# Kernel optimization log

Hardware: AMD Instinct MI355X
Metric: run time of the kernel (lower is better)

Reference implementation:

```python
import jax, jax.numpy as jnp
import numpy as np

N = 100000      # nodes
E = 1600000     # edges
IN_DIM = 256
HID = 64
NCLS = 32


def setup_inputs() -> dict:
    key = jax.random.key(0)
    ks = jax.random.split(key, 7)
    features = jax.random.normal(ks[0], (N, IN_DIM), dtype=jnp.float32)
    hidden_prev = jax.random.normal(ks[1], (N, HID), dtype=jnp.float32)
    adj_indices = jax.random.randint(ks[2], (2, E), 0, N, dtype=jnp.int32)
    # torch.rand init, scaled by 0.1 to keep activations numerically sane
    W0 = jax.random.uniform(ks[3], (IN_DIM, HID), dtype=jnp.float32) * 0.1
    W1 = jax.random.uniform(ks[4], (HID, HID), dtype=jnp.float32) * 0.1
    W2 = jax.random.uniform(ks[5], (HID, NCLS), dtype=jnp.float32) * 0.1
    att_w = jax.random.uniform(ks[6], (2 * HID, 1), dtype=jnp.float32) * 0.1
    return {"features": features, "hidden_prev": hidden_prev,
            "adj_indices": adj_indices, "W0": W0, "W1": W1, "W2": W2,
            "att_w": att_w}


def _edge_softmax(scores, rows, n):
    # sparse softmax over dim=1 of an NxN COO: normalize per source row
    m = jax.ops.segment_max(scores, rows, num_segments=n)
    ex = jnp.exp(scores - m[rows])
    s = jax.ops.segment_sum(ex, rows, num_segments=n)
    return ex / s[rows]


def _compute_attention(hfeat, adj_indices, att_w):
    src, dst = adj_indices[0], adj_indices[1]
    h = hfeat.shape[1]
    # cat(f_src, f_dst) @ att_w == f_src @ w_a + f_dst @ w_b ; project per-node
    proj_a = hfeat @ att_w[:h, 0]   # [N]
    proj_b = hfeat @ att_w[h:, 0]   # [N]
    scores = jax.nn.leaky_relu(proj_a[src] + proj_b[dst])  # [E]
    return _edge_softmax(scores, src, hfeat.shape[0])


def _spmm(att_vals, adj_indices, x):
    # out[i] = sum_{(i,j) in E} att * x[j]
    src, dst = adj_indices[0], adj_indices[1]
    return jax.ops.segment_sum(att_vals[:, None] * x[dst], src,
                               num_segments=x.shape[0])


def reference(features, hidden_prev, adj_indices, W0, W1, W2, att_w):
    att = _compute_attention(hidden_prev, adj_indices, att_w)  # [E]
    h = features
    for W in (W0, W1, W2):
        h = jax.nn.elu(_spmm(att, adj_indices, h @ W))
    return jax.nn.log_softmax(h, axis=1)
```

## Files before the change

kernel.cpp:

```cpp
#include <hip/hip_runtime.h>
#include <math.h>

#define HIDN 64
#define NCLS_K 32
#define INDIM 256
#define BSHIFT 7
#define MAXBUCK 1024
#define BUCK_CAP 4096
#define DSTBITS 17
#define DSTMASK ((1 << DSTBITS) - 1)
#define SCB 512

typedef unsigned int uint;
typedef unsigned short ushort;
typedef __attribute__((ext_vector_type(8))) short short8v;
typedef __attribute__((ext_vector_type(4))) float f32x4;

__device__ inline ushort f2bf(float f) {
  uint u = __float_as_uint(f);
  return (ushort)((u + 0x7FFFu + ((u >> 16) & 1u)) >> 16);
}
__device__ inline float bf2f(ushort h) { return __uint_as_float(((uint)h) << 16); }

__global__ __launch_bounds__(256) void proj_kernel(const float* __restrict__ hid,
    const float* __restrict__ attw, float* __restrict__ pa, float* __restrict__ pb, int n) {
  int wid  = (blockIdx.x * blockDim.x + threadIdx.x) >> 6;
  int lane = threadIdx.x & 63;
  if (wid >= n) return;
  float v = hid[(size_t)wid * HIDN + lane];
  float a = v * attw[lane];
  float b = v * attw[HIDN + lane];
  #pragma unroll
  for (int off = 32; off >= 1; off >>= 1) {
    a += __shfl_xor(a, off, 64);
    b += __shfl_xor(b, off, 64);
  }
  if (lane == 0) { pa[wid] = a; pb[wid] = b; }
}

__global__ __launch_bounds__(256) void hist2(const int* __restrict__ src,
    int* __restrict__ hmatT, int e, int nb, int nper) {
  __shared__ int h[MAXBUCK];
  int lo = blockIdx.x * nper;
  int hi = min(e, lo + nper);
  for (int j = threadIdx.x; j < nb; j += 256) h[j] = 0;
  __syncthreads();
  for (int i = lo + threadIdx.x; i < hi; i += 256)
    atomicAdd(&h[src[i] >> BSHIFT], 1);
  __syncthreads();
  for (int j = threadIdx.x; j < nb; j += 256)
    hmatT[(size_t)j * SCB + blockIdx.x] = h[j];
}

__global__ __launch_bounds__(256) void col_scan(int* __restrict__ hmatT,
    int* __restrict__ bcnt, int nb) {
  constexpr int PER = SCB / 64;
  int wv = blockIdx.x * 4 + (threadIdx.x >> 6);
  if (wv >= nb) return;
  int lane = threadIdx.x & 63;
  int* col = hmatT + (size_t)wv * SCB + lane * PER;
  int v[PER];
  int s = 0;
  #pragma unroll
  for (int q = 0; q < PER; ++q) { v[q] = col[q]; s += v[q]; }
  int x = s;
  #pragma unroll
  for (int off = 1; off < 64; off <<= 1) {
    int t = __shfl_up(x, off, 64);
    if (lane >= off) x += t;
  }
  int pre = x - s;
  #pragma unroll
  for (int q = 0; q < PER; ++q) { int t = v[q]; col[q] = pre; pre += t; }
  if (lane == 63) bcnt[wv] = pre;
}

__global__ __launch_bounds__(1024) void scan_buckets(const int* __restrict__ bcnt,
    int* __restrict__ bbase, int* __restrict__ rowp, int nb, int n, int e) {
  __shared__ int sm[1024];
  int tid = threadIdx.x;
  int v = (tid < nb) ? bcnt[tid] : 0;
  sm[tid] = v;
  __syncthreads();
  for (int off = 1; off < 1024; off <<= 1) {
    int t = (tid >= off) ? sm[tid - off] : 0;
    __syncthreads();
    sm[tid] += t;
    __syncthreads();
  }
  if (tid < nb) bbase[tid] = sm[tid] - v;
  if (tid == 0) { bbase[nb] = e; rowp[n] = e; }
}

__global__ __launch_bounds__(256) void scatter2(const int* __restrict__ src,
    const int* __restrict__ dst, const int* __restrict__ hmatT,
    const int* __restrict__ bbase, int* __restrict__ pairs, int e, int nb, int nper) {
  __shared__ int h[MAXBUCK];
  int lo = blockIdx.x * nper;
  int hi = min(e, lo + nper);
  for (int j = threadIdx.x; j < nb; j += 256)
    h[j] = bbase[j] + hmatT[(size_t)j * SCB + blockIdx.x];
  __syncthreads();
  for (int i = lo + threadIdx.x; i < hi; i += 256) {
    int s = src[i];
    int pos = atomicAdd(&h[s >> BSHIFT], 1);
    pairs[pos] = ((s & 127) << DSTBITS) | dst[i];
  }
}

__global__ __launch_bounds__(256) void build_csr(const int* __restrict__ pairs,
    const int* __restrict__ bbase, int* __restrict__ rowp,
    int* __restrict__ dstc, int n) {
  __shared__ int hist[128];
  __shared__ int cur[128];
  __shared__ int ord[BUCK_CAP];
  int b = blockIdx.x;
  int tid = threadIdx.x;
  int base = bbase[b];
  int m = bbase[b + 1] - base;
  if (tid < 128) hist[tid] = 0;
  __syncthreads();
  for (int i = tid; i < m; i += 256)
    atomicAdd(&hist[pairs[base + i] >> DSTBITS], 1);
  __syncthreads();
  int own = (tid < 128) ? hist[tid] : 0;
  for (int off = 1; off < 128; off <<= 1) {
    int t = (tid < 128 && tid >= off) ? hist[tid - off] : 0;
    __syncthreads();
    if (tid < 128) hist[tid] += t;
    __syncthreads();
  }
  if (tid < 128) {
    int excl = hist[tid] - own;
    cur[tid] = excl;
    int s = (b << BSHIFT) + tid;
    if (s < n) rowp[s] = base + excl;
  }
  __syncthreads();
  for (int i = tid; i < m; i += 256) {
    int key = pairs[base + i];
    int pos = atomicAdd(&cur[key >> DSTBITS], 1);
    ord[pos] = key;
  }
  __syncthreads();
  for (int i = tid; i < m; i += 256) dstc[base + i] = ord[i];
}

__device__ inline int wave_sort64(int key, int lane) {
  #pragma unroll
  for (int k = 2; k <= 64; k <<= 1) {
    #pragma unroll
    for (int j = k >> 1; j > 0; j >>= 1) {
      int p = __shfl_xor(key, j, 64);
      bool up    = ((lane & k) == 0);
      bool lower = ((lane & j) == 0);
      int mn = min(key, p), mx = max(key, p);
      key = (lower == up) ? mn : mx;
    }
  }
  return key;
}

__global__ __launch_bounds__(256) void att_softmax(const float* __restrict__ pa,
    const float* __restrict__ pb, int* __restrict__ dstc,
    const int* __restrict__ rowp, ushort* __restrict__ attb, int n) {
  int wid  = (blockIdx.x * blockDim.x + threadIdx.x) >> 6;
  int lane = threadIdx.x & 63;
  if (wid >= n) return;
  int start = rowp[wid], end = rowp[wid + 1];
  int c = end - start;
  if (c <= 0) return;
  float pai = pa[wid];
  if (c <= 64) {
    int e = start + lane;
    int key = (lane < c) ? dstc[e] : 0x7FFFFFFF;
    key = wave_sort64(key, lane);
    float s = -3.0e38f;
    if (lane < c) {
      dstc[e] = key;
      float v = pai + pb[key & DSTMASK];
      s = v > 0.f ? v : 0.01f * v;
    }
    float m = s;
    #pragma unroll
    for (int off = 32; off >= 1; off >>= 1) m = fmaxf(m, __shfl_xor(m, off, 64));
    float ex = (lane < c) ? expf(s - m) : 0.f;
    float sum = ex;
    #pragma unroll
    for (int off = 32; off >= 1; off >>= 1) sum += __shfl_xor(sum, off, 64);
    if (lane < c) attb[e] = f2bf(ex / sum);
    return;
  }
  float m = -3.0e38f;
  for (int base = start; base < end; base += 64) {
    int e = base + lane;
    int key = (e < end) ? dstc[e] : 0x7FFFFFFF;
    key = wave_sort64(key, lane);
    float s = -3.0e38f;
    if (e < end) {
      dstc[e] = key;
      float v = pai + pb[key & DSTMASK];
      s = v > 0.f ? v : 0.01f * v;
      attb[e] = f2bf(s);
    }
    m = fmaxf(m, s);
  }
  #pragma unroll
  for (int off = 32; off >= 1; off >>= 1) m = fmaxf(m, __shfl_xor(m, off, 64));
  float sum = 0.f;
  for (int base = start; base < end; base += 64) {
    int e = base + lane;
    float ex = 0.f;
    if (e < end) { ex = expf(bf2f(attb[e]) - m); attb[e] = f2bf(ex); }
    sum += ex;
  }
  #pragma unroll
  for (int off = 32; off >= 1; off >>= 1) sum += __shfl_xor(sum, off, 64);
  float inv = 1.f / sum;
  for (int base = start; base < end; base += 64) {
    int e = base + lane;
    if (e < end) attb[e] = f2bf(bf2f(attb[e]) * inv);
  }
}

template <int K, int TJ>
__global__ __launch_bounds__(256) void gemm_mfma(const float* __restrict__ A,
    const float* __restrict__ W, ushort* __restrict__ Xb, int n) {
  constexpr int KP = K + 8;
  constexpr int NCB = TJ / 16;
  __shared__ ushort Wt[TJ][KP];
  const int tid = threadIdx.x;
  for (int idx = tid; idx < K * TJ; idx += 256) {
    int k = idx / TJ, j = idx % TJ;
    Wt[j][k] = f2bf(W[idx]);
  }
  __syncthreads();
  const int wv   = blockIdx.x * 4 + (tid >> 6);
  const int row0 = wv * 16;
  if (row0 >= n) return;
  const int lane = tid & 63;
  const int r    = lane & 15;
  const int kg   = lane >> 4;
  const int rowA = min(row0 + r, n - 1);
  const float* ap = A + (size_t)rowA * K + kg * 8;

  f32x4 acc[NCB];
  #pragma unroll
  for (int c = 0; c < NCB; ++c) acc[c] = (f32x4)(0.f);

  #pragma unroll
  for (int ks = 0; ks < K / 32; ++ks) {
    float4 a0 = *reinterpret_cast<const float4*>(ap + ks * 32);
    float4 a1 = *reinterpret_cast<const float4*>(ap + ks * 32 + 4);
    union { short8v v; ushort u[8]; } af;
    af.u[0] = f2bf(a0.x); af.u[1] = f2bf(a0.y);
    af.u[2] = f2bf(a0.z); af.u[3] = f2bf(a0.w);
    af.u[4] = f2bf(a1.x); af.u[5] = f2bf(a1.y);
    af.u[6] = f2bf(a1.z); af.u[7] = f2bf(a1.w);
    #pragma unroll
    for (int c = 0; c < NCB; ++c) {
      short8v bf = *reinterpret_cast<const short8v*>(&Wt[c * 16 + r][ks * 32 + kg * 8]);
      acc[c] = __builtin_amdgcn_mfma_f32_16x16x32_bf16(af.v, bf, acc[c], 0, 0, 0);
    }
  }
  #pragma unroll
  for (int c = 0; c < NCB; ++c) {
    #pragma unroll
    for (int i = 0; i < 4; ++i) {
      int rowS = row0 + kg * 4 + i;
      if (rowS < n) Xb[(size_t)rowS * TJ + c * 16 + r] = f2bf(acc[c][i]);
    }
  }
}

template <int TJ, bool FINAL>
__global__ __launch_bounds__(256) void spmm_mfma(const ushort* __restrict__ Xb,
    const ushort* __restrict__ attb, const int* __restrict__ dstc,
    const int* __restrict__ rowp, float* __restrict__ out, int n) {
  constexpr int NCB = TJ / 16;
  constexpr int CH  = TJ / 8;
  constexpr int EPP = 64 / CH;
  constexpr int RS  = TJ + 4;
  __shared__ ushort Xs[4][32 * RS];
  const int tid   = threadIdx.x;
  const int wslot = tid >> 6;
  const int g     = blockIdx.x * 4 + wslot;
  const int row0  = g * 16;
  if (row0 >= n) return;
  const int lane = tid & 63;
  const int r    = lane & 15;
  const int kg   = lane >> 4;
  const int start = rowp[row0];
  const int end   = rowp[min(row0 + 16, n)];
  ushort* xs = Xs[wslot];
  const int cg = lane % CH;
  const int ce = lane / CH;

  f32x4 acc[NCB];
  #pragma unroll
  for (int c = 0; c < NCB; ++c) acc[c] = (f32x4)(0.f);

  for (int base = start; base < end; base += 32) {
    #pragma unroll
    for (int p = 0; p < CH / 2; ++p) {
      int el  = p * EPP + ce;
      int idx = min(base + el, end - 1);
      int d   = dstc[idx] & DSTMASK;
      uint4 u = *reinterpret_cast<const uint4*>(Xb + (size_t)d * TJ + cg * 8);
      *reinterpret_cast<uint4*>(&xs[el * RS + cg * 8]) = u;
    }
    int sbase = base + 8 * kg;
    union { short8v v; ushort u[8]; } af;
    #pragma unroll
    for (int j = 0; j < 8; ++j) {
      int e = sbase + j;
      bool valid = e < end;
      int idx = valid ? e : (end - 1);
      int v = dstc[idx];
      ushort a = attb[idx];
      int rid = (v >> DSTBITS) & 15;
      af.u[j] = (valid && rid == r) ? a : (ushort)0;
    }
    #pragma unroll
    for (int c = 0; c < NCB; ++c) {
      union { short8v v; ushort u[8]; } bf;
      #pragma unroll
      for (int i = 0; i < 8; ++i)
        bf.u[i] = xs[(8 * kg + i) * RS + c * 16 + r];
      acc[c] = __builtin_amdgcn_mfma_f32_16x16x32_bf16(af.v, bf.v, acc[c], 0, 0, 0);
    }
  }
  #pragma unroll
  for (int c = 0; c < NCB; ++c)
    #pragma unroll
    for (int i = 0; i < 4; ++i)
      acc[c][i] = acc[c][i] > 0.f ? acc[c][i] : (expf(acc[c][i]) - 1.f);
  if (!FINAL) {
    #pragma unroll
    for (int c = 0; c < NCB; ++c)
      #pragma unroll
      for (int i = 0; i < 4; ++i) {
        int rowS = row0 + kg * 4 + i;
        if (rowS < n) out[(size_t)rowS * TJ + c * 16 + r] = acc[c][i];
      }
  } else {
    #pragma unroll
    for (int i = 0; i < 4; ++i) {
      float m = acc[0][i];
      #pragma unroll
      for (int c = 1; c < NCB; ++c) m = fmaxf(m, acc[c][i]);
      #pragma unroll
      for (int off = 1; off < 16; off <<= 1) m = fmaxf(m, __shfl_xor(m, off));
      float s = 0.f;
      #pragma unroll
      for (int c = 0; c < NCB; ++c) s += expf(acc[c][i] - m);
      #pragma unroll
      for (int off = 1; off < 16; off <<= 1) s += __shfl_xor(s, off);
      float lg = m + logf(s);
      int rowS = row0 + kg * 4 + i;
      if (rowS < n) {
        #pragma unroll
        for (int c = 0; c < NCB; ++c)
          out[(size_t)rowS * TJ + c * 16 + r] = acc[c][i] - lg;
      }
    }
  }
}

extern "C" void kernel_launch(void* const* d_in, const int* in_sizes, int n_in,
                              void* d_out, int out_size, void* d_ws, size_t ws_size,
                              hipStream_t stream) {
  const float* features = (const float*)d_in[0];
  const float* hidden   = (const float*)d_in[1];
  const int*   adj      = (const int*)d_in[2];
  const float* W0       = (const float*)d_in[3];
  const float* W1       = (const float*)d_in[4];
  const float* W2       = (const float*)d_in[5];
  const float* attw     = (const float*)d_in[6];
  float* out = (float*)d_out;

  const int N = in_sizes[1] / HIDN;
  const int E = in_sizes[2] / 2;
  const int* src = adj;
  const int* dst = adj + E;
  const int NBUCK = (N + 127) >> BSHIFT;
  const int NB2   = ((NBUCK + 15) / 16) * 16;
  const int nper  = (E + SCB - 1) / SCB;

  int*   rowp  = (int*)d_ws;
  int*   bbase = rowp + (N + 16);
  int*   bcnt  = bbase + (NB2 + 16);
  int*   hmatT = bcnt + NB2;
  int*   dstc  = hmatT + (size_t)NBUCK * SCB;
  ushort* attb = (ushort*)(dstc + E);
  float* Xf    = (float*)(attb) + (E / 2 + 16);
  float* H     = Xf + (size_t)N * HIDN;
  ushort* Xb   = (ushort*)Xf;
  int*   pairs = (int*)Xf;
  float* pa    = H;
  float* pb    = H + N;

  dim3 blk(256);
  const int gridWave = (N + 3) / 4;
  const int gridG16  = ((N + 15) / 16 + 3) / 4;

  proj_kernel<<<gridWave, blk, 0, stream>>>(hidden, attw, pa, pb, N);
  hist2<<<SCB, blk, 0, stream>>>(src, hmatT, E, NBUCK, nper);
  col_scan<<<(NBUCK + 3) / 4, blk, 0, stream>>>(hmatT, bcnt, NBUCK);
  scan_buckets<<<1, 1024, 0, stream>>>(bcnt, bbase, rowp, NBUCK, N, E);
  scatter2<<<SCB, blk, 0, stream>>>(src, dst, hmatT, bbase, pairs, E, NBUCK, nper);
  build_csr<<<NBUCK, blk, 0, stream>>>(pairs, bbase, rowp, dstc, N);
  att_softmax<<<gridWave, blk, 0, stream>>>(pa, pb, dstc, rowp, attb, N);

  gemm_mfma<INDIM, HIDN><<<gridG16, blk, 0, stream>>>(features, W0, Xb, N);
  spmm_mfma<HIDN, false><<<gridG16, blk, 0, stream>>>(Xb, attb, dstc, rowp, H, N);
  gemm_mfma<HIDN, HIDN><<<gridG16, blk, 0, stream>>>(H, W1, Xb, N);
  spmm_mfma<HIDN, false><<<gridG16, blk, 0, stream>>>(Xb, attb, dstc, rowp, H, N);
  gemm_mfma<HIDN, NCLS_K><<<gridG16, blk, 0, stream>>>(H, W2, Xb, N);
  spmm_mfma<NCLS_K, true><<<gridG16, blk, 0, stream>>>(Xb, attb, dstc, rowp, out, N);
}
```

Before: 301.0 us.

## Interleave edges per 16-row group and software-pipeline SpMM gathers

Adds a reorder16 kernel that permutes each 16-row group's edges into round-robin order across rows, so each 32-edge chunk spreads evenly over the rows the MFMA tile covers. The SpMM kernel now loads the keys and attention values for a chunk once per lane and broadcasts them with shuffles instead of reloading them per element. It also prefetches the next chunk's gathered feature rows into registers while the current chunk computes. The cost is an extra pass over the edge arrays and higher register pressure. The reorder skips groups whose row degree reaches 64 or whose edge count exceeds 768.

```diff
diff --git a/kernel.cpp b/kernel.cpp
--- a/kernel.cpp
+++ b/kernel.cpp
@@ -223,6 +223,59 @@
   }
 }
 
+__global__ __launch_bounds__(256) void reorder16(int* __restrict__ dstc,
+    ushort* __restrict__ attb, const int* __restrict__ rowp, int n) {
+  int g = blockIdx.x * 4 + (threadIdx.x >> 6);
+  int row0 = g * 16;
+  if (row0 >= n) return;
+  int lane = threadIdx.x & 63;
+  int nr = min(16, n - row0);
+  int start = rowp[row0];
+  int end   = rowp[row0 + nr];
+  int m = end - start;
+  if (m <= 0) return;
+  int myd = (lane < nr) ? (rowp[row0 + lane + 1] - rowp[row0 + lane]) : 0;
+  int maxd = myd;
+  #pragma unroll
+  for (int off = 32; off >= 1; off >>= 1) maxd = max(maxd, __shfl_xor(maxd, off, 64));
+  if (maxd > 63 || m > 12 * 64) return;
+  int cnt = 0;
+  #pragma unroll
+  for (int rr = 0; rr < 16; ++rr) cnt += (__shfl(myd, rr, 64) > lane) ? 1 : 0;
+  int C = cnt;
+  #pragma unroll
+  for (int off = 1; off < 64; off <<= 1) {
+    int t = __shfl_up(C, off, 64);
+    if (lane >= off) C += t;
+  }
+  C -= cnt;
+  int key[12]; ushort av[12]; int pos[12]; bool val[12];
+  #pragma unroll
+  for (int q = 0; q < 12; ++q) {
+    int i = start + lane + q * 64;
+    val[q] = (i < end);
+    int ic = val[q] ? i : start;
+    int k = dstc[ic];
+    av[q] = attb[ic];
+    int r = (k >> DSTBITS) & 15;
+    int j = (ic - rowp[row0 + r]) & 63;
+    int rank = 0;
+    #pragma unroll
+    for (int rp = 0; rp < 16; ++rp) {
+      int drp = __shfl(myd, rp, 64);
+      rank += (rp < r && drp > j) ? 1 : 0;
+    }
+    int Cj = __shfl(C, j, 64);
+    key[q] = k;
+    pos[q] = start + Cj + rank;
+  }
+  asm volatile("s_waitcnt vmcnt(0)" ::: "memory");
+  #pragma unroll
+  for (int q = 0; q < 12; ++q) {
+    if (val[q]) { dstc[pos[q]] = key[q]; attb[pos[q]] = av[q]; }
+  }
+}
+
 template <int K, int TJ>
 __global__ __launch_bounds__(256) void gemm_mfma(const float* __restrict__ A,
     const float* __restrict__ W, ushort* __restrict__ Xb, int n) {
@@ -279,6 +332,7 @@
     const int* __restrict__ rowp, float* __restrict__ out, int n) {
   constexpr int NCB = TJ / 16;
   constexpr int CH  = TJ / 8;
+  constexpr int CHH = CH / 2;
   constexpr int EPP = 64 / CH;
   constexpr int RS  = TJ + 4;
   __shared__ ushort Xs[4][32 * RS];
@@ -293,33 +347,51 @@
   const int start = rowp[row0];
   const int end   = rowp[min(row0 + 16, n)];
   ushort* xs = Xs[wslot];
-  const int cg = lane % CH;
-  const int ce = lane / CH;
+  const int cg  = lane % CH;
+  const int ce  = lane / CH;
+  const int l31 = lane & 31;
 
   f32x4 acc[NCB];
   #pragma unroll
   for (int c = 0; c < NCB; ++c) acc[c] = (f32x4)(0.f);
 
+  int k32 = 0, a32 = 0;
+  uint4 pre[CHH];
+  if (start < end) {
+    k32 = dstc[min(start + l31, end - 1)];
+    a32 = (int)attb[min(start + l31, end - 1)];
+    #pragma unroll
+    for (int p = 0; p < CHH; ++p) {
+      int el = p * EPP + ce;
+      int d  = __shfl(k32, el, 64) & DSTMASK;
+      pre[p] = *reinterpret_cast<const uint4*>(Xb + (size_t)d * TJ + cg * 8);
+    }
+  }
   for (int base = start; base < end; base += 32) {
-    #pragma unroll
-    for (int p = 0; p < CH / 2; ++p) {
-      int el  = p * EPP + ce;
-      int idx = min(base + el, end - 1);
-      int d   = dstc[idx] & DSTMASK;
-      uint4 u = *reinterpret_cast<const uint4*>(Xb + (size_t)d * TJ + cg * 8);
-      *reinterpret_cast<uint4*>(&xs[el * RS + cg * 8]) = u;
-    }
-    int sbase = base + 8 * kg;
+    int nb = (base + 32 < end) ? base + 32 : base;
+    int nk = dstc[min(nb + l31, end - 1)];
+    int na = (int)attb[min(nb + l31, end - 1)];
+    uint4 nxt[CHH];
+    #pragma unroll
+    for (int p = 0; p < CHH; ++p) {
+      int el = p * EPP + ce;
+      int d  = __shfl(nk, el, 64) & DSTMASK;
+      nxt[p] = *reinterpret_cast<const uint4*>(Xb + (size_t)d * TJ + cg * 8);
+    }
+    #pragma unroll
+    for (int p = 0; p < CHH; ++p) {
+      int el = p * EPP + ce;
+      *reinterpret_cast<uint4*>(&xs[el * RS + cg * 8]) = pre[p];
+    }
+    int sj = 8 * kg;
     union { short8v v; ushort u[8]; } af;
     #pragma unroll
     for (int j = 0; j < 8; ++j) {
-      int e = sbase + j;
-      bool valid = e < end;
-      int idx = valid ? e : (end - 1);
-      int v = dstc[idx];
-      ushort a = attb[idx];
-      int rid = (v >> DSTBITS) & 15;
-      af.u[j] = (valid && rid == r) ? a : (ushort)0;
+      int kk = __shfl(k32, sj + j, 64);
+      int aa = __shfl(a32, sj + j, 64);
+      bool valid = (base + sj + j) < end;
+      int rid = (kk >> DSTBITS) & 15;
+      af.u[j] = (valid && rid == r) ? (ushort)aa : (ushort)0;
     }
     #pragma unroll
     for (int c = 0; c < NCB; ++c) {
@@ -329,6 +401,9 @@
         bf.u[i] = xs[(8 * kg + i) * RS + c * 16 + r];
       acc[c] = __builtin_amdgcn_mfma_f32_16x16x32_bf16(af.v, bf.v, acc[c], 0, 0, 0);
     }
+    k32 = nk; a32 = na;
+    #pragma unroll
+    for (int p = 0; p < CHH; ++p) pre[p] = nxt[p];
   }
   #pragma unroll
   for (int c = 0; c < NCB; ++c)
@@ -411,6 +486,7 @@
   scatter2<<<SCB, blk, 0, stream>>>(src, dst, hmatT, bbase, pairs, E, NBUCK, nper);
   build_csr<<<NBUCK, blk, 0, stream>>>(pairs, bbase, rowp, dstc, N);
   att_softmax<<<gridWave, blk, 0, stream>>>(pa, pb, dstc, rowp, attb, N);
+  reorder16<<<gridG16, blk, 0, stream>>>(dstc, attb, rowp, N);
 
   gemm_mfma<INDIM, HIDN><<<gridG16, blk, 0, stream>>>(features, W0, Xb, N);
   spmm_mfma<HIDN, false><<<gridG16, blk, 0, stream>>>(Xb, attb, dstc, rowp, H, N);
```

New measurement: 463.1 us. 53.8% more time.

## Interleave CSR entries within 16-row groups for balanced SpMM access

Applied to the files above, without the earlier changes.

Adds a kernel that permutes each 16-row group's edge list (packed dst keys and bf16 attention values) into a round-robin order across rows, using prefix counts of per-row degrees. The aim is that the SpMM kernel, which reads a group's edges as one range, sees lanes spread evenly across rows with better coalescing. It costs an extra pass over the edge arrays, and groups with high-degree rows are skipped.

```diff
diff --git a/kernel.cpp b/kernel.cpp
--- a/kernel.cpp
+++ b/kernel.cpp
@@ -220,6 +220,59 @@
   for (int base = start; base < end; base += 64) {
     int e = base + lane;
     if (e < end) attb[e] = f2bf(bf2f(attb[e]) * inv);
+  }
+}
+
+__global__ __launch_bounds__(256) void reorder16(int* __restrict__ dstc,
+    ushort* __restrict__ attb, const int* __restrict__ rowp, int n) {
+  int g = blockIdx.x * 4 + (threadIdx.x >> 6);
+  int row0 = g * 16;
+  if (row0 >= n) return;
+  int lane = threadIdx.x & 63;
+  int nr = min(16, n - row0);
+  int start = rowp[row0];
+  int end   = rowp[row0 + nr];
+  int m = end - start;
+  if (m <= 0) return;
+  int myd = (lane < nr) ? (rowp[row0 + lane + 1] - rowp[row0 + lane]) : 0;
+  int maxd = myd;
+  #pragma unroll
+  for (int off = 32; off >= 1; off >>= 1) maxd = max(maxd, __shfl_xor(maxd, off, 64));
+  if (maxd > 63 || m > 12 * 64) return;
+  int cnt = 0;
+  #pragma unroll
+  for (int rr = 0; rr < 16; ++rr) cnt += (__shfl(myd, rr, 64) > lane) ? 1 : 0;
+  int C = cnt;
+  #pragma unroll
+  for (int off = 1; off < 64; off <<= 1) {
+    int t = __shfl_up(C, off, 64);
+    if (lane >= off) C += t;
+  }
+  C -= cnt;
+  int key[12]; ushort av[12]; int pos[12]; bool val[12];
+  #pragma unroll
+  for (int q = 0; q < 12; ++q) {
+    int i = start + lane + q * 64;
+    val[q] = (i < end);
+    int ic = val[q] ? i : start;
+    int k = dstc[ic];
+    av[q] = attb[ic];
+    int r = (k >> DSTBITS) & 15;
+    int j = (ic - rowp[row0 + r]) & 63;
+    int rank = 0;
+    #pragma unroll
+    for (int rp = 0; rp < 16; ++rp) {
+      int drp = __shfl(myd, rp, 64);
+      rank += (rp < r && drp > j) ? 1 : 0;
+    }
+    int Cj = __shfl(C, j, 64);
+    key[q] = k;
+    pos[q] = start + Cj + rank;
+  }
+  asm volatile("s_waitcnt vmcnt(0)" ::: "memory");
+  #pragma unroll
+  for (int q = 0; q < 12; ++q) {
+    if (val[q]) { dstc[pos[q]] = key[q]; attb[pos[q]] = av[q]; }
   }
 }
 
@@ -411,6 +464,7 @@
   scatter2<<<SCB, blk, 0, stream>>>(src, dst, hmatT, bbase, pairs, E, NBUCK, nper);
   build_csr<<<NBUCK, blk, 0, stream>>>(pairs, bbase, rowp, dstc, N);
   att_softmax<<<gridWave, blk, 0, stream>>>(pa, pb, dstc, rowp, attb, N);
+  reorder16<<<gridG16, blk, 0, stream>>>(dstc, attb, rowp, N);
 
   gemm_mfma<INDIM, HIDN><<<gridG16, blk, 0, stream>>>(features, W0, Xb, N);
   spmm_mfma<HIDN, false><<<gridG16, blk, 0, stream>>>(Xb, attb, dstc, rowp, H, N);
```

After: 294.1 us. 2.3% less time.
